# Kernel tuning notes

Hardware: AMD Instinct MI355X
Metric: run time of the kernel (lower is better)

Reference implementation:

```python
import jax, jax.numpy as jnp
import numpy as np

B, S, D, H = 2, 2048, 1024, 16
HD = D // H  # head_dim = 64


def setup_inputs() -> dict:
    key = jax.random.key(0)
    ks = jax.random.split(key, 10)
    std = 1.0 / np.sqrt(D)
    inputs = jax.random.normal(ks[0], (B, S, D), dtype=jnp.float32)
    # stacked per-head projection weights: [H, HD, D] (row-major like nn.Linear)
    Wq = jax.random.uniform(ks[1], (H, HD, D), jnp.float32, -std, std)
    bq = jax.random.uniform(ks[2], (H, HD), jnp.float32, -std, std)
    Wk = jax.random.uniform(ks[3], (H, HD, D), jnp.float32, -std, std)
    bk = jax.random.uniform(ks[4], (H, HD), jnp.float32, -std, std)
    Wv = jax.random.uniform(ks[5], (H, HD, D), jnp.float32, -std, std)
    bv = jax.random.uniform(ks[6], (H, HD), jnp.float32, -std, std)
    Wo = jax.random.uniform(ks[7], (D, D), jnp.float32, -std, std)
    bo = jax.random.uniform(ks[8], (D,), jnp.float32, -std, std)
    return {"inputs": inputs, "Wq": Wq, "bq": bq, "Wk": Wk, "bk": bk,
            "Wv": Wv, "bv": bv, "Wo": Wo, "bo": bo}


def reference(inputs, Wq, bq, Wk, bk, Wv, bv, Wo, bo):
    # per-head projections, batched over heads: [B,H,S,HD]
    q = jnp.einsum('bsd,hed->bhse', inputs, Wq) + bq[None, :, None, :]
    k = jnp.einsum('bsd,hed->bhse', inputs, Wk) + bk[None, :, None, :]
    v = jnp.einsum('bsd,hed->bhse', inputs, Wv) + bv[None, :, None, :]
    scale = 1.0 / np.sqrt(HD).astype(np.float32)
    # explicit [B,H,S,S] score matrix, as in the original naive attention
    scores = jnp.einsum('bhqe,bhke->bhqk', q, k) * scale
    causal = jnp.tril(jnp.ones((S, S), dtype=bool))
    scores = jnp.where(causal[None, None], scores, jnp.float32(-jnp.inf))
    attn = jax.nn.softmax(scores, axis=-1)  # dropout p=0 -> identity
    wv = jnp.einsum('bhqk,bhke->bhqe', attn, v)
    # concat heads along feature dim: [B,S,H*HD] = [B,S,D]
    z = wv.transpose(0, 2, 1, 3).reshape(B, S, D)
    out = jnp.einsum('bsd,ed->bse', z, Wo) + bo
    return out
```

## Files before the change

### kernel.cpp

```cpp
#include <hip/hip_runtime.h>
#include <math.h>

#define Bx 2
#define Sx 2048
#define Dx 1024
#define Hx 16
#define HDx 64
#define Mx (Bx*Sx)

typedef __bf16 bf16x8 __attribute__((ext_vector_type(8)));
typedef __bf16 bf16x4 __attribute__((ext_vector_type(4)));
typedef float  f32x4  __attribute__((ext_vector_type(4)));

#define SCL 0.18033688011112042f

__device__ __forceinline__ void gload_lds16(const __bf16* g, __bf16* l) {
  __builtin_amdgcn_global_load_lds(
      (const __attribute__((address_space(1))) unsigned int*)g,
      (__attribute__((address_space(3))) unsigned int*)l, 16, 0, 0);
}

__device__ __forceinline__ void cvt8(const float* s, __bf16* d) {
  float4 a = *(const float4*)s;
  float4 b = *(const float4*)(s + 4);
  bf16x8 o;
  o[0] = (__bf16)a.x; o[1] = (__bf16)a.y; o[2] = (__bf16)a.z; o[3] = (__bf16)a.w;
  o[4] = (__bf16)b.x; o[5] = (__bf16)b.y; o[6] = (__bf16)b.z; o[7] = (__bf16)b.w;
  *(bf16x8*)d = o;
}

__global__ __launch_bounds__(256) void cvt_kernel(
    const float* __restrict__ x, const float* __restrict__ Wq,
    const float* __restrict__ Wk, const float* __restrict__ Wv,
    const float* __restrict__ Wo, const float* __restrict__ bq,
    const float* __restrict__ bk, const float* __restrict__ bv,
    __bf16* __restrict__ xb, __bf16* __restrict__ wqkv,
    __bf16* __restrict__ wob, float* __restrict__ bqkv)
{
  const int bid = blockIdx.x;
  const int t = threadIdx.x;
  const size_t MEG = 1024u * 1024u;
  if (bid < 2048) {
    size_t e = (size_t)bid * 2048 + t * 8;
    cvt8(x + e, xb + e);
  } else if (bid < 3584) {
    size_t e = (size_t)(bid - 2048) * 2048 + t * 8;
    const float* src = (e < MEG) ? (Wq + e) : (e < 2 * MEG) ? (Wk + (e - MEG)) : (Wv + (e - 2 * MEG));
    cvt8(src, wqkv + e);
  } else if (bid < 4096) {
    size_t e = (size_t)(bid - 3584) * 2048 + t * 8;
    cvt8(Wo + e, wob + e);
  } else {
    for (int i = t; i < 3072; i += 256)
      bqkv[i] = (i < 1024) ? bq[i] : (i < 2048) ? bk[i - 1024] : bv[i - 2048];
  }
}

template<int TM, int TN, int MODE>
__global__ __launch_bounds__(256) void gemm_k(
    const __bf16* __restrict__ A, const __bf16* __restrict__ W,
    const float* __restrict__ bias, float* __restrict__ Cf,
    __bf16* __restrict__ Cb, __bf16* __restrict__ vT,
    int M, int N, int K, int ldc)
{
  __shared__ __align__(16) char smem[2 * (TM + TN) * 64 * 2];
  __bf16* AsB = (__bf16*)smem;

  constexpr int MS = TM / 32;
  constexpr int NS = TN / 32;
  const int tid = threadIdx.x;
  const int lane = tid & 63, wave = tid >> 6;
  const int l16 = lane & 15, quad = lane >> 4;
  const int wm = (wave >> 1) * (TM / 2);
  const int wn = (wave & 1) * (TN / 2);
  const int swz = l16 & 7;

  const int lid = blockIdx.y * gridDim.x + blockIdx.x;
  const int g8 = lid >> 6;
  const int r64 = lid & 63;
  const int gpm = (int)gridDim.y >> 3;
  const int gm = g8 % gpm;
  const int gn = g8 / gpm;
  const int m0 = (gm * 8 + (r64 & 7)) * TM;
  const int n0 = (gn * 8 + (r64 >> 3)) * TN;

  const f32x4 zero = {0.f, 0.f, 0.f, 0.f};
  f32x4 acc[MS][NS];
#pragma unroll
  for (int i = 0; i < MS; ++i)
#pragma unroll
    for (int j = 0; j < NS; ++j) acc[i][j] = zero;

  const int srow = tid >> 3;
  const int scs = (tid & 7) ^ (srow & 7);
  const __bf16* Ag = A + (size_t)(m0 + srow) * K + scs * 8;
  const __bf16* Wg = W + (size_t)(n0 + srow) * K + scs * 8;

#define G_STAGE(k0_, b_)                                                        \
  { __bf16* As_ = AsB + (b_) * (TM + TN) * 64;                                  \
    __bf16* Bs_ = As_ + TM * 64;                                                \
    _Pragma("unroll")                                                           \
    for (int i = 0; i < TM / 32; ++i)                                           \
      gload_lds16(Ag + (size_t)(i * 32) * K + (k0_), &As_[(i * 256 + tid) * 8]);\
    _Pragma("unroll")                                                           \
    for (int i = 0; i < TN / 32; ++i)                                           \
      gload_lds16(Wg + (size_t)(i * 32) * K + (k0_), &Bs_[(i * 256 + tid) * 8]); }

  const int NT = K >> 6;
  G_STAGE(0, 0)
  __syncthreads();

  for (int t = 0; t < NT; ++t) {
    if (t + 1 < NT) G_STAGE((t + 1) << 6, (t + 1) & 1)
    const __bf16* As_ = AsB + (t & 1) * (TM + TN) * 64;
    const __bf16* Bs_ = As_ + TM * 64;
#pragma unroll
    for (int hk = 0; hk < 2; ++hk) {
      const int ph = ((hk * 4 + quad) ^ swz) * 8;
      bf16x8 af[MS], bfr[NS];
#pragma unroll
      for (int i = 0; i < MS; ++i)
        af[i] = *(const bf16x8*)&As_[(wm + i * 16 + l16) * 64 + ph];
#pragma unroll
      for (int j = 0; j < NS; ++j)
        bfr[j] = *(const bf16x8*)&Bs_[(wn + j * 16 + l16) * 64 + ph];
#pragma unroll
      for (int i = 0; i < MS; ++i)
#pragma unroll
        for (int j = 0; j < NS; ++j)
          acc[i][j] = __builtin_amdgcn_mfma_f32_16x16x32_bf16(af[i], bfr[j], acc[i][j], 0, 0, 0);
    }
    __syncthreads();
  }

  if (MODE == 0) {
    float* Cs = (float*)smem;
    constexpr int cst = TN + 4;
#pragma unroll
    for (int j = 0; j < NS; ++j) {
      const int c = wn + j * 16 + l16;
      const float bv_ = bias[n0 + c];
#pragma unroll
      for (int i = 0; i < MS; ++i) {
        const int r0 = wm + i * 16 + quad * 4;
#pragma unroll
        for (int g = 0; g < 4; ++g)
          Cs[(r0 + g) * cst + c] = acc[i][j][g] + bv_;
      }
    }
    __syncthreads();
    constexpr int passes = TM * TN / (256 * 4);
#pragma unroll
    for (int p = 0; p < passes; ++p) {
      const int slot = p * 256 + tid;
      const int row = slot / (TN / 4);
      const int col4 = (slot % (TN / 4)) * 4;
      f32x4 v = *(const f32x4*)&Cs[row * cst + col4];
      *(f32x4*)&Cf[(size_t)(m0 + row) * ldc + n0 + col4] = v;
    }
  } else {
    __bf16* Cs = (__bf16*)smem;
    constexpr int cst = TN + 8;
    const bool vtile = (n0 >= 2048);
    if (!vtile) {
#pragma unroll
      for (int j = 0; j < NS; ++j) {
        const int c = wn + j * 16 + l16;
        const float bv_ = bias[n0 + c];
        const float sc = ((n0 + c) < 1024) ? SCL : 1.0f;
#pragma unroll
        for (int i = 0; i < MS; ++i) {
          const int r0 = wm + i * 16 + quad * 4;
#pragma unroll
          for (int g = 0; g < 4; ++g)
            Cs[(r0 + g) * cst + c] = (__bf16)((acc[i][j][g] + bv_) * sc);
        }
      }
      __syncthreads();
      constexpr int passes = TM * TN / (256 * 8);
#pragma unroll
      for (int p = 0; p < passes; ++p) {
        const int slot = p * 256 + tid;
        const int row = slot / (TN / 8);
        const int col8 = (slot % (TN / 8)) * 8;
        bf16x8 v = *(const bf16x8*)&Cs[row * cst + col8];
        *(bf16x8*)&Cb[(size_t)(m0 + row) * 3072 + n0 + col8] = v;
      }
    } else {
      constexpr int cstT = TM + 8;
#pragma unroll
      for (int j = 0; j < NS; ++j) {
        const int c = wn + j * 16 + l16;
        const float bv_ = bias[n0 + c];
#pragma unroll
        for (int i = 0; i < MS; ++i) {
          const int r0 = wm + i * 16 + quad * 4;
#pragma unroll
          for (int g = 0; g < 4; ++g)
            Cs[c * cstT + r0 + g] = (__bf16)(acc[i][j][g] + bv_);
        }
      }
      __syncthreads();
      const int bb = m0 >> 11, ml = m0 & 2047;
      constexpr int passes = TM * TN / (256 * 8);
#pragma unroll
      for (int p = 0; p < passes; ++p) {
        const int slot = p * 256 + tid;
        const int dd = slot / (TM / 8);
        const int ss8 = (slot % (TM / 8)) * 8;
        bf16x8 v = *(const bf16x8*)&Cs[dd * cstT + ss8];
        const int c2 = n0 - 2048 + dd;
        const int hh = c2 >> 6, ddd = c2 & 63;
        *(bf16x8*)&vT[((size_t)(bb * 16 + hh) * 64 + ddd) * 2048 + ml + ss8] = v;
      }
    }
  }
}

__global__ __launch_bounds__(256, 4) void attn_mfma(
    const __bf16* __restrict__ qkv, const __bf16* __restrict__ vT,
    __bf16* __restrict__ zb)
{
  __shared__ __bf16 Qs[64 * 64];
  __shared__ __bf16 Ks[2][64 * 64];
  __shared__ __bf16 Vs[2][64 * 64];

  const int tid = threadIdx.x;
  const int lane = tid & 63, wave = tid >> 6;
  const int l16 = lane & 15, quad = lane >> 4;
  const int bx = blockIdx.x;
  const int bh = bx & 31;
  const int s8 = (bx >> 5) & 7;
  const int p4 = bx >> 8;
  const int qt = (p4 == 0) ? s8 : (p4 == 1) ? 15 - s8 : (p4 == 2) ? 16 + s8 : 31 - s8;
  const int h = bh & 15, b = bh >> 4;
  const int q0 = qt * 64;

  const __bf16* qg = qkv + (size_t)b * 2048 * 3072 + h * 64;
  const __bf16* kg = qg + 1024;
  const __bf16* vg = vT + (size_t)bh * 64 * 2048;

#define STAGE_K(kt_, kbuf)                                                      \
  { const int kn = (kt_) * 64;                                                  \
    _Pragma("unroll")                                                           \
    for (int i = 0; i < 2; ++i) {                                               \
      int slot = i * 256 + tid;                                                 \
      int row = slot >> 3, ph2 = slot & 7;                                      \
      int cs = ph2 ^ (row & 7);                                                 \
      gload_lds16(kg + (size_t)(kn + row) * 3072 + cs * 8, &Ks[kbuf][slot * 8]);\
    } }

#define STAGE_V(kt_, vbuf)                                                      \
  { const int kn = (kt_) * 64;                                                  \
    _Pragma("unroll")                                                           \
    for (int i = 0; i < 2; ++i) {                                               \
      int slot = i * 256 + tid;                                                 \
      int row = slot >> 3, ph2 = slot & 7;                                      \
      int cs = ph2 ^ (row & 7);                                                 \
      gload_lds16(vg + (size_t)row * 2048 + kn + cs * 8, &Vs[vbuf][slot * 8]);  \
    } }

#pragma unroll
  for (int i = 0; i < 2; ++i) {
    int slot = i * 256 + tid;
    int row = slot >> 3, ph2 = slot & 7;
    int cs = ph2 ^ (row & 7);
    gload_lds16(qg + (size_t)(q0 + row) * 3072 + cs * 8, &Qs[slot * 8]);
  }
  STAGE_K(0, 0)
  STAGE_V(0, 0)
  __syncthreads();

  const int swz = l16 & 7;
  const int sw0 = ((quad) ^ swz) * 8;
  const int sw1 = ((quad + 4) ^ swz) * 8;

  bf16x8 qf0[4], qf1[4];
#pragma unroll
  for (int n = 0; n < 4; ++n) {
    qf0[n] = *(const bf16x8*)&Qs[(n * 16 + l16) * 64 + sw0];
    qf1[n] = *(const bf16x8*)&Qs[(n * 16 + l16) * 64 + sw1];
  }
  __bf16* Pf = Qs;
  __bf16* P = &Qs[wave * 16 * 64];

  bf16x8 onesf;
  {
    __bf16 ov = (l16 == 0) ? (__bf16)1.0f : (__bf16)0.0f;
#pragma unroll
    for (int i = 0; i < 8; ++i) onesf[i] = ov;
  }

  const f32x4 zero = {0.f, 0.f, 0.f, 0.f};
  f32x4 O[4], Ol = zero;
#pragma unroll
  for (int j = 0; j < 4; ++j) O[j] = zero;
  f32x4 s_cur[4], s_next[4];

#define S_TILE(sdst, kb)                                                        \
  { __builtin_amdgcn_s_setprio(1);                                              \
    bf16x8 kf0 = *(const bf16x8*)&Ks[kb][(wave * 16 + l16) * 64 + sw0];         \
    bf16x8 kf1 = *(const bf16x8*)&Ks[kb][(wave * 16 + l16) * 64 + sw1];         \
    _Pragma("unroll")                                                           \
    for (int n = 0; n < 4; ++n) {                                               \
      sdst[n] = zero;                                                           \
      sdst[n] = __builtin_amdgcn_mfma_f32_16x16x32_bf16(kf0, qf0[n], sdst[n],0,0,0);\
      sdst[n] = __builtin_amdgcn_mfma_f32_16x16x32_bf16(kf1, qf1[n], sdst[n],0,0,0);\
    }                                                                           \
    __builtin_amdgcn_s_setprio(0); }

#define EXP_P(s, DIAG)                                                          \
  { _Pragma("unroll")                                                           \
    for (int n = 0; n < 4; ++n) {                                               \
      const int ql = n * 16 + l16;                                              \
      bf16x4 st;                                                                \
      _Pragma("unroll")                                                         \
      for (int g = 0; g < 4; ++g) {                                             \
        float p = __builtin_exp2f(s[n][g]);                                     \
        if (DIAG && (wave * 16 + quad * 4 + g) > ql) p = 0.f;                   \
        st[g] = (__bf16)p;                                                      \
      }                                                                         \
      *(bf16x4*)&Pf[ql * 64 + (((2 * wave + (quad >> 1)) ^ swz) * 8) + (quad & 1) * 4] = st; \
    } }

#define PV_TILE(vb)                                                             \
  { bf16x8 pf0 = *(const bf16x8*)&P[l16 * 64 + sw0];                            \
    bf16x8 pf1 = *(const bf16x8*)&P[l16 * 64 + sw1];                            \
    __builtin_amdgcn_s_setprio(1);                                              \
    _Pragma("unroll")                                                           \
    for (int j = 0; j < 4; ++j) {                                               \
      bf16x8 vf0 = *(const bf16x8*)&Vs[vb][(j * 16 + l16) * 64 + sw0];          \
      O[j] = __builtin_amdgcn_mfma_f32_16x16x32_bf16(pf0, vf0, O[j], 0, 0, 0);  \
      bf16x8 vf1 = *(const bf16x8*)&Vs[vb][(j * 16 + l16) * 64 + sw1];          \
      O[j] = __builtin_amdgcn_mfma_f32_16x16x32_bf16(pf1, vf1, O[j], 0, 0, 0);  \
    }                                                                           \
    Ol = __builtin_amdgcn_mfma_f32_16x16x32_bf16(pf0, onesf, Ol, 0, 0, 0);      \
    Ol = __builtin_amdgcn_mfma_f32_16x16x32_bf16(pf1, onesf, Ol, 0, 0, 0);      \
    __builtin_amdgcn_s_setprio(0); }

  STAGE_K(1, 1)
  S_TILE(s_cur, 0)
  __syncthreads();

  for (int t = 0; t < qt; ++t) {
    STAGE_V(t + 1, (t + 1) & 1)
    if (t + 2 <= qt) STAGE_K(t + 2, t & 1)
    EXP_P(s_cur, false)
    S_TILE(s_next, (t + 1) & 1)
    __syncthreads();
    PV_TILE(t & 1)
    __syncthreads();
#pragma unroll
    for (int n = 0; n < 4; ++n) s_cur[n] = s_next[n];
  }
  EXP_P(s_cur, true)
  __syncthreads();
  PV_TILE(qt & 1)

  const int rq = q0 + wave * 16 + quad * 4;
#pragma unroll
  for (int g = 0; g < 4; ++g) {
    const float lv = __shfl(Ol[g], quad * 16);
    const float inv = 1.0f / lv;
    const size_t rb = (size_t)(b * 2048 + rq + g) * 1024 + h * 64 + l16;
#pragma unroll
    for (int j = 0; j < 4; ++j)
      zb[rb + j * 16] = (__bf16)(O[j][g] * inv);
  }
}

extern "C" void kernel_launch(void* const* d_in, const int* in_sizes, int n_in,
                              void* d_out, int out_size, void* d_ws, size_t ws_size,
                              hipStream_t stream) {
  (void)in_sizes; (void)n_in; (void)out_size; (void)ws_size;
  const float* x  = (const float*)d_in[0];
  const float* Wq = (const float*)d_in[1];
  const float* bq = (const float*)d_in[2];
  const float* Wk = (const float*)d_in[3];
  const float* bk = (const float*)d_in[4];
  const float* Wv = (const float*)d_in[5];
  const float* bv = (const float*)d_in[6];
  const float* Wo = (const float*)d_in[7];
  const float* bo = (const float*)d_in[8];

  char* ws = (char*)d_ws;
  __bf16* xb   = (__bf16*)(ws);
  __bf16* wqkv = (__bf16*)(ws + (8ull  << 20));
  __bf16* wob  = (__bf16*)(ws + (14ull << 20));
  float*  bqkv = (float*) (ws + (16ull << 20));
  __bf16* qkv  = (__bf16*)(ws + (17ull << 20));
  __bf16* vT   = (__bf16*)(ws + (41ull << 20));
  __bf16* zb   = (__bf16*)(ws + (49ull << 20));

  cvt_kernel<<<4097, 256, 0, stream>>>(x, Wq, Wk, Wv, Wo, bq, bk, bv,
                                       xb, wqkv, wob, bqkv);
  gemm_k<128, 128, 1><<<dim3(24, 32), 256, 0, stream>>>(
      xb, wqkv, bqkv, nullptr, qkv, vT, Mx, 3072, 1024, 0);
  attn_mfma<<<1024, 256, 0, stream>>>(qkv, vT, zb);
  gemm_k<128, 64, 0><<<dim3(16, 32), 256, 0, stream>>>(
      zb, wob, bo, (float*)d_out, nullptr, nullptr, Mx, 1024, 1024, 1024);
}
```

Measured before the change: 179.1 us.

## Keep P in registers and split PV over keys with cross-wave reduction

The attention kernel no longer writes the exponentiated scores to LDS for the PV product. Each wave keeps its own P fragment in registers, zero-padded to the MFMA K width, and accumulates a partial O over its own 16-key slice. The four partial outputs and row sums are then combined through LDS at the end. This removes one barrier and the P LDS round trip per tile, but half of each PV MFMA multiplies zero padding and the accumulators grow to 64 floats per lane. The change also reorders the tile schedule to run the heaviest query tiles first and lowers the occupancy hint from 4 to 3.

Result: no change. 178.7 us (median of 2 runs) (-0.2%).

```diff
diff --git a/kernel.cpp b/kernel.cpp
--- a/kernel.cpp
+++ b/kernel.cpp
@@ -217,7 +217,7 @@
   }
 }
 
-__global__ __launch_bounds__(256, 4) void attn_mfma(
+__global__ __launch_bounds__(256, 3) void attn_mfma(
     const __bf16* __restrict__ qkv, const __bf16* __restrict__ vT,
     __bf16* __restrict__ zb)
 {
@@ -229,10 +229,8 @@
   const int lane = tid & 63, wave = tid >> 6;
   const int l16 = lane & 15, quad = lane >> 4;
   const int bx = blockIdx.x;
+  const int qt = 31 - (bx >> 5);
   const int bh = bx & 31;
-  const int s8 = (bx >> 5) & 7;
-  const int p4 = bx >> 8;
-  const int qt = (p4 == 0) ? s8 : (p4 == 1) ? 15 - s8 : (p4 == 2) ? 16 + s8 : 31 - s8;
   const int h = bh & 15, b = bh >> 4;
   const int q0 = qt * 64;
 
@@ -274,6 +272,8 @@
   const int swz = l16 & 7;
   const int sw0 = ((quad) ^ swz) * 8;
   const int sw1 = ((quad + 4) ^ swz) * 8;
+  const int vcol = (((2 * wave + (quad >> 1)) ^ swz) * 8) + (quad & 1) * 4;
+  const __bf16 ZB = (__bf16)0.0f;
 
   bf16x8 qf0[4], qf1[4];
 #pragma unroll
@@ -281,91 +281,136 @@
     qf0[n] = *(const bf16x8*)&Qs[(n * 16 + l16) * 64 + sw0];
     qf1[n] = *(const bf16x8*)&Qs[(n * 16 + l16) * 64 + sw1];
   }
-  __bf16* Pf = Qs;
-  __bf16* P = &Qs[wave * 16 * 64];
-
-  bf16x8 onesf;
-  {
-    __bf16 ov = (l16 == 0) ? (__bf16)1.0f : (__bf16)0.0f;
-#pragma unroll
-    for (int i = 0; i < 8; ++i) onesf[i] = ov;
-  }
 
   const f32x4 zero = {0.f, 0.f, 0.f, 0.f};
-  f32x4 O[4], Ol = zero;
-#pragma unroll
-  for (int j = 0; j < 4; ++j) O[j] = zero;
-  f32x4 s_cur[4], s_next[4];
-
-#define S_TILE(sdst, kb)                                                        \
+  f32x4 acc[4][4];
+#pragma unroll
+  for (int jt = 0; jt < 4; ++jt)
+#pragma unroll
+    for (int n = 0; n < 4; ++n) acc[jt][n] = zero;
+  float lacc[4] = {0.f, 0.f, 0.f, 0.f};
+  f32x4 s[4];
+  bf16x8 pb[4];
+
+#define S_TILE(kb)                                                              \
   { __builtin_amdgcn_s_setprio(1);                                              \
     bf16x8 kf0 = *(const bf16x8*)&Ks[kb][(wave * 16 + l16) * 64 + sw0];         \
     bf16x8 kf1 = *(const bf16x8*)&Ks[kb][(wave * 16 + l16) * 64 + sw1];         \
     _Pragma("unroll")                                                           \
     for (int n = 0; n < 4; ++n) {                                               \
-      sdst[n] = zero;                                                           \
-      sdst[n] = __builtin_amdgcn_mfma_f32_16x16x32_bf16(kf0, qf0[n], sdst[n],0,0,0);\
-      sdst[n] = __builtin_amdgcn_mfma_f32_16x16x32_bf16(kf1, qf1[n], sdst[n],0,0,0);\
+      s[n] = zero;                                                              \
+      s[n] = __builtin_amdgcn_mfma_f32_16x16x32_bf16(kf0, qf0[n], s[n], 0, 0, 0);\
+      s[n] = __builtin_amdgcn_mfma_f32_16x16x32_bf16(kf1, qf1[n], s[n], 0, 0, 0);\
     }                                                                           \
     __builtin_amdgcn_s_setprio(0); }
 
-#define EXP_P(s, DIAG)                                                          \
+  const int kqb = wave * 16 + quad * 4;
+
+#define EXP_PB(DIAG)                                                            \
   { _Pragma("unroll")                                                           \
     for (int n = 0; n < 4; ++n) {                                               \
       const int ql = n * 16 + l16;                                              \
-      bf16x4 st;                                                                \
+      float e0 = __builtin_exp2f(s[n][0]);                                      \
+      float e1 = __builtin_exp2f(s[n][1]);                                      \
+      float e2 = __builtin_exp2f(s[n][2]);                                      \
+      float e3 = __builtin_exp2f(s[n][3]);                                      \
+      if (DIAG) {                                                               \
+        if (kqb + 0 > ql) e0 = 0.f;                                             \
+        if (kqb + 1 > ql) e1 = 0.f;                                             \
+        if (kqb + 2 > ql) e2 = 0.f;                                             \
+        if (kqb + 3 > ql) e3 = 0.f;                                             \
+      }                                                                         \
+      pb[n] = (bf16x8){(__bf16)e0, (__bf16)e1, (__bf16)e2, (__bf16)e3,          \
+                       ZB, ZB, ZB, ZB};                                         \
+      lacc[n] += (e0 + e1) + (e2 + e3);                                         \
+    } }
+
+#define PV_TILE(vb)                                                             \
+  { __builtin_amdgcn_s_setprio(1);                                              \
+    _Pragma("unroll")                                                           \
+    for (int jt = 0; jt < 4; ++jt) {                                            \
+      bf16x4 vv = *(const bf16x4*)&Vs[vb][(jt * 16 + l16) * 64 + vcol];         \
+      bf16x8 av = (bf16x8){vv[0], vv[1], vv[2], vv[3], ZB, ZB, ZB, ZB};         \
       _Pragma("unroll")                                                         \
-      for (int g = 0; g < 4; ++g) {                                             \
-        float p = __builtin_exp2f(s[n][g]);                                     \
-        if (DIAG && (wave * 16 + quad * 4 + g) > ql) p = 0.f;                   \
-        st[g] = (__bf16)p;                                                      \
-      }                                                                         \
-      *(bf16x4*)&Pf[ql * 64 + (((2 * wave + (quad >> 1)) ^ swz) * 8) + (quad & 1) * 4] = st; \
-    } }
-
-#define PV_TILE(vb)                                                             \
-  { bf16x8 pf0 = *(const bf16x8*)&P[l16 * 64 + sw0];                            \
-    bf16x8 pf1 = *(const bf16x8*)&P[l16 * 64 + sw1];                            \
-    __builtin_amdgcn_s_setprio(1);                                              \
-    _Pragma("unroll")                                                           \
-    for (int j = 0; j < 4; ++j) {                                               \
-      bf16x8 vf0 = *(const bf16x8*)&Vs[vb][(j * 16 + l16) * 64 + sw0];          \
-      O[j] = __builtin_amdgcn_mfma_f32_16x16x32_bf16(pf0, vf0, O[j], 0, 0, 0);  \
-      bf16x8 vf1 = *(const bf16x8*)&Vs[vb][(j * 16 + l16) * 64 + sw1];          \
-      O[j] = __builtin_amdgcn_mfma_f32_16x16x32_bf16(pf1, vf1, O[j], 0, 0, 0);  \
+      for (int n = 0; n < 4; ++n)                                               \
+        acc[jt][n] = __builtin_amdgcn_mfma_f32_16x16x32_bf16(av, pb[n], acc[jt][n], 0, 0, 0); \
     }                                                                           \
-    Ol = __builtin_amdgcn_mfma_f32_16x16x32_bf16(pf0, onesf, Ol, 0, 0, 0);      \
-    Ol = __builtin_amdgcn_mfma_f32_16x16x32_bf16(pf1, onesf, Ol, 0, 0, 0);      \
     __builtin_amdgcn_s_setprio(0); }
 
   STAGE_K(1, 1)
-  S_TILE(s_cur, 0)
+  S_TILE(0)
   __syncthreads();
 
   for (int t = 0; t < qt; ++t) {
+    EXP_PB(false)
     STAGE_V(t + 1, (t + 1) & 1)
     if (t + 2 <= qt) STAGE_K(t + 2, t & 1)
-    EXP_P(s_cur, false)
-    S_TILE(s_next, (t + 1) & 1)
-    __syncthreads();
+    S_TILE((t + 1) & 1)
     PV_TILE(t & 1)
     __syncthreads();
-#pragma unroll
-    for (int n = 0; n < 4; ++n) s_cur[n] = s_next[n];
-  }
-  EXP_P(s_cur, true)
-  __syncthreads();
+  }
+  EXP_PB(true)
   PV_TILE(qt & 1)
-
-  const int rq = q0 + wave * 16 + quad * 4;
-#pragma unroll
-  for (int g = 0; g < 4; ++g) {
-    const float lv = __shfl(Ol[g], quad * 16);
-    const float inv = 1.0f / lv;
-    const size_t rb = (size_t)(b * 2048 + rq + g) * 1024 + h * 64 + l16;
-#pragma unroll
-    for (int j = 0; j < 4; ++j)
-      zb[rb + j * 16] = (__bf16)(O[j][g] * inv);
+  __syncthreads();
+
+  float* redA = (float*)&Ks[0][0];
+  float* redB = (float*)&Vs[0][0];
+  float* lred = (float*)Qs;
+#pragma unroll
+  for (int n = 0; n < 4; ++n) {
+    float v = lacc[n];
+    v += __shfl_xor(v, 16);
+    v += __shfl_xor(v, 32);
+    lacc[n] = v;
+  }
+  if (quad == 0) {
+#pragma unroll
+    for (int n = 0; n < 4; ++n) lred[wave * 64 + n * 16 + l16] = lacc[n];
+  }
+
+#define WR_ACC(dst)                                                             \
+  { _Pragma("unroll")                                                           \
+    for (int jt = 0; jt < 4; ++jt)                                              \
+      _Pragma("unroll")                                                         \
+      for (int n = 0; n < 4; ++n)                                               \
+        *(f32x4*)&dst[(jt * 4 + n) * 256 + lane * 4] = acc[jt][n]; }
+#define ADD_ACC(srcp)                                                           \
+  { _Pragma("unroll")                                                           \
+    for (int jt = 0; jt < 4; ++jt)                                              \
+      _Pragma("unroll")                                                         \
+      for (int n = 0; n < 4; ++n) {                                             \
+        f32x4 tmp = *(const f32x4*)&srcp[(jt * 4 + n) * 256 + lane * 4];        \
+        acc[jt][n] += tmp;                                                      \
+      } }
+
+  if (wave == 1) WR_ACC(redA)
+  if (wave == 3) WR_ACC(redB)
+  __syncthreads();
+  if (wave == 0) ADD_ACC(redA)
+  if (wave == 2) ADD_ACC(redB)
+  __syncthreads();
+  if (wave == 2) WR_ACC(redA)
+  __syncthreads();
+  if (wave == 0) {
+    ADD_ACC(redA)
+    float inv[4];
+#pragma unroll
+    for (int n = 0; n < 4; ++n) {
+      const float lsum = lred[n * 16 + l16] + lred[64 + n * 16 + l16]
+                       + lred[128 + n * 16 + l16] + lred[192 + n * 16 + l16];
+      inv[n] = 1.0f / lsum;
+    }
+#pragma unroll
+    for (int jt = 0; jt < 4; ++jt)
+#pragma unroll
+      for (int n = 0; n < 4; ++n) {
+        bf16x4 ov = (bf16x4){(__bf16)(acc[jt][n][0] * inv[n]),
+                             (__bf16)(acc[jt][n][1] * inv[n]),
+                             (__bf16)(acc[jt][n][2] * inv[n]),
+                             (__bf16)(acc[jt][n][3] * inv[n])};
+        *(bf16x4*)&zb[(size_t)(b * 2048 + q0 + n * 16 + l16) * 1024
+                      + h * 64 + jt * 16 + quad * 4] = ov;
+      }
   }
 }
 
```
